# Optimization experiments

Hardware: AMD Instinct MI355X
Metric: run time of the kernel (lower is better)

Reference implementation:

```python
import jax, jax.numpy as jnp
import numpy as np

DIM = 1536; NH = 12; HD = 128; C2 = HD // 2          # rope half-dim = 64
F, H, W = 1, 30, 52
FRAME = H * W                                         # 1560 tokens/frame
SINK_FRAMES = 1; LOCAL_ATTN = 6
SINK = SINK_FRAMES * FRAME                            # 1560
MAX_ATTN = LOCAL_ATTN * 1560                          # 9360
CACHE = 9360                                          # kv cache length
GLOBAL_END = 9360; LOCAL_END_CACHE = 9360             # cache state before step
SPLITS = (C2 - 2 * (C2 // 3), C2 // 3, C2 // 3)       # (22, 21, 21)
EPS = 1e-6


def setup_inputs() -> dict:
    key = jax.random.key(0)
    ks = jax.random.split(key, 12)
    s = F * H * W
    rn = lambda k, sh, sc=1.0: jax.random.normal(k, sh, jnp.float32) * sc
    x = rn(ks[0], (1, s, DIM))
    Wq = rn(ks[1], (DIM, DIM), 0.02); Wk = rn(ks[2], (DIM, DIM), 0.02)
    Wv = rn(ks[3], (DIM, DIM), 0.02); Wo = rn(ks[4], (DIM, DIM), 0.02)
    zb = jnp.zeros((DIM,), jnp.float32)
    angles = jax.random.uniform(ks[5], (1024, C2), jnp.float32) * (2.0 * np.pi)
    freqs_cos = jnp.cos(angles); freqs_sin = jnp.sin(angles)
    cache_k = rn(ks[6], (1, CACHE, NH, HD)); cache_v = rn(ks[7], (1, CACHE, NH, HD))
    return dict(x=x, Wq=Wq, bq=zb, Wk=Wk, bk=zb, Wv=Wv, bv=zb, Wo=Wo, bo=zb,
                nq_w=jnp.ones((DIM,), jnp.float32), nk_w=jnp.ones((DIM,), jnp.float32),
                cache_k=cache_k, cache_v=cache_v,
                freqs_cos=freqs_cos, freqs_sin=freqs_sin,
                seq_lens=jnp.array([s], jnp.int32),
                grid_sizes=jnp.array([[F, H, W]], jnp.int32),
                current_start=GLOBAL_END)


def _rmsnorm(x, w):
    return x * jax.lax.rsqrt(jnp.mean(x * x, -1, keepdims=True) + EPS) * w


def _grid_table(table, start_frame):
    """table [1024, C2] -> per-token rope factors [S, 1, C2] over the (F,H,W) grid."""
    s0, s1, s2 = SPLITS
    tf, th, tw = table[:, :s0], table[:, s0:s0 + s1], table[:, s0 + s1:]
    fp = jnp.broadcast_to(tf[start_frame:start_frame + F][:, None, None, :], (F, H, W, s0))
    hp = jnp.broadcast_to(th[:H][None, :, None, :], (F, H, W, s1))
    wp = jnp.broadcast_to(tw[:W][None, None, :, :], (F, H, W, s2))
    return jnp.concatenate([fp, hp, wp], -1).reshape(F * H * W, 1, C2)


def _rope(x, cos, sin):
    # x: [b, s, n, d]; cos/sin: [s, 1, C2] (complex multiply in real arithmetic)
    b, s, n, d = x.shape
    xp = x.reshape(b, s, n, d // 2, 2)
    xr, xi = xp[..., 0], xp[..., 1]
    c, sn = cos[None], sin[None]                      # [1, s, 1, C2]
    out_r = xr * c - xi * sn
    out_i = xr * sn + xi * c
    return jnp.stack([out_r, out_i], -1).reshape(b, s, n, d)


def reference(x, Wq, bq, Wk, bk, Wv, bv, Wo, bo, nq_w, nk_w,
              cache_k, cache_v, freqs_cos, freqs_sin,
              seq_lens, grid_sizes, current_start):
    b, s = x.shape[:2]
    q = _rmsnorm(x @ Wq.T + bq, nq_w).reshape(b, s, NH, HD)
    k = _rmsnorm(x @ Wk.T + bk, nk_w).reshape(b, s, NH, HD)
    v = (x @ Wv.T + bv).reshape(b, s, NH, HD)

    start_frame = int(current_start) // FRAME
    cos = _grid_table(freqs_cos, start_frame)
    sin = _grid_table(freqs_sin, start_frame)
    rq = _rope(q, cos, sin)
    rk = _rope(k, cos, sin)

    # --- static cache bookkeeping (roll_and_insert path; all Python ints) ---
    num_new = s
    current_end = int(current_start) + num_new
    num_evicted = num_new + LOCAL_END_CACHE - CACHE           # 1560
    num_rolled = LOCAL_END_CACHE - num_evicted - SINK         # 6240
    local_end = LOCAL_END_CACHE + current_end - GLOBAL_END - num_evicted  # 9360
    local_start = local_end - num_new                         # 7800 == SINK + num_rolled
    temp_k = jnp.concatenate(
        [cache_k[:, :SINK], cache_k[:, SINK + num_evicted:SINK + num_evicted + num_rolled], rk], axis=1)
    temp_v = jnp.concatenate(
        [cache_v[:, :SINK], cache_v[:, SINK + num_evicted:SINK + num_evicted + num_rolled], v], axis=1)

    # --- sink + sliding-window attention ---
    local_budget = MAX_ATTN - SINK
    win_start = max(SINK, local_end - local_budget)
    k_cat = jnp.concatenate([temp_k[:, :SINK], temp_k[:, win_start:local_end]], axis=1)
    v_cat = jnp.concatenate([temp_v[:, :SINK], temp_v[:, win_start:local_end]], axis=1)

    logits = jnp.einsum('bqhd,bkhd->bhqk', rq, k_cat) * (HD ** -0.5)
    probs = jax.nn.softmax(logits, axis=-1)
    out = jnp.einsum('bhqk,bkhd->bqhd', probs, v_cat)
    y = out.reshape(b, s, DIM) @ Wo.T + bo
    return y
```

## Files before the change

kernel.cpp:

```cpp
#include <hip/hip_runtime.h>
#include <hip/hip_bf16.h>

typedef __bf16 bf16;
typedef __bf16 bf16x2 __attribute__((ext_vector_type(2)));
typedef __bf16 bf16x4 __attribute__((ext_vector_type(4)));
typedef __bf16 bf16x8 __attribute__((ext_vector_type(8)));
typedef float f32x4 __attribute__((ext_vector_type(4)));

#define DIM 1536
#define NH 12
#define HD 128
#define SEQ 1560
#define KV 9360
#define KVP 9408
#define SINK 1560
#define NEWBASE 7800
#define QSCALE 0.08838834764831845f
#define NSPLIT 3
#define CHUNK 3136

__device__ __forceinline__ void gl_lds16(const void* g, void* l) {
  __builtin_amdgcn_global_load_lds(
      (const __attribute__((address_space(1))) unsigned int*)g,
      (__attribute__((address_space(3))) unsigned int*)l, 16, 0, 0);
}

__global__ __launch_bounds__(256) void castk(const float* __restrict__ src,
                                             bf16* __restrict__ dst, int n) {
  int i = (blockIdx.x * 256 + threadIdx.x) * 8;
  if (i < n) {
    float4 a = *(const float4*)(src + i);
    float4 b = *(const float4*)(src + i + 4);
    bf16x8 o;
    o[0] = (bf16)a.x; o[1] = (bf16)a.y; o[2] = (bf16)a.z; o[3] = (bf16)a.w;
    o[4] = (bf16)b.x; o[5] = (bf16)b.y; o[6] = (bf16)b.z; o[7] = (bf16)b.w;
    *(bf16x8*)(dst + i) = o;
  }
}

struct GemmBatch {
  const bf16* B[3];
  const float* bias[3];
  float* C[3];
};

#define BM 128
#define BN 128
#define BK 32

__global__ __launch_bounds__(256, 2) void gemm_bt(const bf16* __restrict__ A,
                                                  GemmBatch gb, int M) {
  const bf16* Bw = gb.B[blockIdx.z];
  const float* bias = gb.bias[blockIdx.z];
  float* C = gb.C[blockIdx.z];
  int bm = blockIdx.x * BM;
  int bn = blockIdx.y * BN;

  __shared__ bf16 Alds[2][BM][BK];
  __shared__ bf16 Blds[2][BN][BK];

  int t = threadIdx.x;
  int lane = t & 63;
  int wave = t >> 6;
  int wr = wave >> 1, wc = wave & 1;
  int fr = lane & 15;
  int fo = (lane >> 4) * 8;

  f32x4 acc[4][4] = {};

  const int NK = DIM / BK;
  int colA = (lane & 3) * 8;
  int lrow = lane >> 2;

#define STAGE(buf, k0)                                                      \
  {                                                                         \
    _Pragma("unroll") for (int p = 0; p < 2; ++p) {                         \
      int rbase = wave * 16 + p * 64;                                       \
      int ga = bm + rbase + lrow;                                           \
      if (ga > M - 1) ga = M - 1;                                           \
      gl_lds16(A + (size_t)ga * DIM + (k0) + colA, &Alds[buf][rbase][0]);   \
      int gbv = bn + rbase + lrow;                                          \
      gl_lds16(Bw + (size_t)gbv * DIM + (k0) + colA, &Blds[buf][rbase][0]); \
    }                                                                       \
  }

  STAGE(0, 0);
  int cur = 0;
  for (int ks = 0; ks < NK; ++ks) {
    __syncthreads();
    if (ks + 1 < NK) STAGE(cur ^ 1, (ks + 1) * BK);
    bf16x8 af[4], bfv[4];
#pragma unroll
    for (int i = 0; i < 4; ++i)
      af[i] = *(const bf16x8*)&Alds[cur][wr * 64 + i * 16 + fr][fo];
#pragma unroll
    for (int j = 0; j < 4; ++j)
      bfv[j] = *(const bf16x8*)&Blds[cur][wc * 64 + j * 16 + fr][fo];
#pragma unroll
    for (int i = 0; i < 4; ++i)
#pragma unroll
      for (int j = 0; j < 4; ++j)
        acc[i][j] = __builtin_amdgcn_mfma_f32_16x16x32_bf16(af[i], bfv[j],
                                                            acc[i][j], 0, 0, 0);
    cur ^= 1;
  }
#undef STAGE

  int g4 = (lane >> 4) * 4;
#pragma unroll
  for (int i = 0; i < 4; ++i) {
    int mbase = bm + wr * 64 + i * 16 + g4;
#pragma unroll
    for (int j = 0; j < 4; ++j) {
      int col = bn + wc * 64 + j * 16 + fr;
      float bv = bias[col];
#pragma unroll
      for (int r = 0; r < 4; ++r) {
        int m = mbase + r;
        if (m < M) C[(size_t)m * DIM + col] = acc[i][j][r] + bv;
      }
    }
  }
}

__global__ __launch_bounds__(256) void norm_rope(
    const float* __restrict__ qraw, const float* __restrict__ kraw,
    const float* __restrict__ nqw, const float* __restrict__ nkw,
    const float* __restrict__ fcos, const float* __restrict__ fsin,
    bf16* __restrict__ Qh, bf16* __restrict__ Kcat) {
  int tok = blockIdx.x;
  int tid = threadIdx.x;
  const float* qr = qraw + (size_t)tok * DIM;
  const float* kr = kraw + (size_t)tok * DIM;
  float sq = 0.f, sk = 0.f;
  for (int c = tid; c < DIM; c += 256) {
    float a = qr[c];
    sq += a * a;
    float b = kr[c];
    sk += b * b;
  }
#pragma unroll
  for (int off = 32; off; off >>= 1) {
    sq += __shfl_down(sq, off);
    sk += __shfl_down(sk, off);
  }
  __shared__ float red[2][4];
  int w = tid >> 6;
  if ((tid & 63) == 0) {
    red[0][w] = sq;
    red[1][w] = sk;
  }
  __syncthreads();
  sq = red[0][0] + red[0][1] + red[0][2] + red[0][3];
  sk = red[1][0] + red[1][1] + red[1][2] + red[1][3];
  float rsq = rsqrtf(sq * (1.0f / DIM) + 1e-6f);
  float rsk = rsqrtf(sk * (1.0f / DIM) + 1e-6f);

  int hrow = tok / 52, wrow = tok % 52;
  for (int p = tid; p < NH * 64; p += 256) {
    int n = p >> 6, i = p & 63;
    int trow = (i < 22) ? 6 : (i < 43 ? hrow : wrow);
    float cs = fcos[trow * 64 + i];
    float sn = fsin[trow * 64 + i];
    int c = n * HD + 2 * i;
    float xr = qr[c] * rsq * nqw[c];
    float xi = qr[c + 1] * rsq * nqw[c + 1];
    bf16x2 qo;
    qo[0] = (bf16)((xr * cs - xi * sn) * QSCALE);
    qo[1] = (bf16)((xr * sn + xi * cs) * QSCALE);
    *(bf16x2*)(Qh + ((size_t)n * SEQ + tok) * HD + 2 * i) = qo;
    float yr = kr[c] * rsk * nkw[c];
    float yi = kr[c + 1] * rsk * nkw[c + 1];
    bf16x2 ko;
    ko[0] = (bf16)(yr * cs - yi * sn);
    ko[1] = (bf16)(yr * sn + yi * cs);
    *(bf16x2*)(Kcat + ((size_t)n * KVP + NEWBASE + tok) * HD + 2 * i) = ko;
  }
}

__global__ __launch_bounds__(256) void build_kcat(const float* __restrict__ cache_k,
                                                  bf16* __restrict__ Kcat) {
  int j = blockIdx.x;
  int src = j < SINK ? j : j + SINK;
  const float* sp = cache_k + (size_t)src * DIM;
  for (int c4 = threadIdx.x; c4 < DIM / 4; c4 += 256) {
    float4 v = *(const float4*)(sp + c4 * 4);
    int c = c4 * 4;
    int n = c >> 7, d = c & 127;
    bf16x4 o;
    o[0] = (bf16)v.x; o[1] = (bf16)v.y; o[2] = (bf16)v.z; o[3] = (bf16)v.w;
    *(bf16x4*)(Kcat + ((size_t)n * KVP + j) * HD + d) = o;
  }
}

__global__ __launch_bounds__(256) void build_vt(const float* __restrict__ cache_v,
                                                const float* __restrict__ vraw,
                                                bf16* __restrict__ Vt) {
  int h = blockIdx.y;
  int j0 = blockIdx.x * 64;
  __shared__ bf16 T[128][72];
  int tid = threadIdx.x;
  for (int idx = tid; idx < 64 * 32; idx += 256) {
    int jl = idx >> 5, s = idx & 31;
    int j = j0 + jl;
    if (j >= KV) continue;
    const float* sp;
    if (j < NEWBASE) {
      int srcj = j < SINK ? j : j + SINK;
      sp = cache_v + (size_t)srcj * DIM + h * HD;
    } else {
      sp = vraw + (size_t)(j - NEWBASE) * DIM + h * HD;
    }
    float4 v = *(const float4*)(sp + s * 4);
    T[s * 4 + 0][jl] = (bf16)v.x;
    T[s * 4 + 1][jl] = (bf16)v.y;
    T[s * 4 + 2][jl] = (bf16)v.z;
    T[s * 4 + 3][jl] = (bf16)v.w;
  }
  __syncthreads();
  for (int idx = tid; idx < 128 * 16; idx += 256) {
    int d = idx >> 4, g = idx & 15;
    int j = j0 + g * 4;
    if (j + 4 > KV) continue;
    bf16x4 o;
    o[0] = T[d][4 * g];
    o[1] = T[d][4 * g + 1];
    o[2] = T[d][4 * g + 2];
    o[3] = T[d][4 * g + 3];
    *(bf16x4*)(Vt + ((size_t)h * HD + d) * KVP + j) = o;
  }
}

__global__ __launch_bounds__(256, 4) void attn_split(const bf16* __restrict__ Qh,
                                                     const bf16* __restrict__ Kcat,
                                                     const bf16* __restrict__ Vt,
                                                     float* __restrict__ Opart,
                                                     float* __restrict__ MLpart) {
  int orig = blockIdx.x;
  int xcd = orig & 7, jj = orig >> 3;
  int wgid = (xcd < 4 ? xcd * 113 : 452 + (xcd - 4) * 112) + jj;
  int qt = wgid % 25;
  int h = (wgid / 25) % NH;
  int sp = wgid / 300;
  int q0 = qt * 64;
  int c0 = sp * CHUNK;

  int t = threadIdx.x, lane = t & 63, w = t >> 6;
  int g = lane >> 4, fr = lane & 15, s3 = fr & 7;

  __shared__ bf16 Klds[64][128];
  __shared__ bf16 Vlds[128][64];
  __shared__ bf16 Plds[4][16][64];

  int qrow = q0 + w * 16 + fr;
  int qcl = qrow < SEQ ? qrow : SEQ - 1;
  const bf16* Qp = Qh + ((size_t)h * SEQ + qcl) * HD + g * 8;
  bf16x8 qf[4];
#pragma unroll
  for (int fk = 0; fk < 4; ++fk) qf[fk] = *(const bf16x8*)(Qp + 32 * fk);

  int kadd[4], vadd[4];
#pragma unroll
  for (int p = 0; p < 4; ++p) {
    int m = (4 * w + p) * 64 + lane;
    int rK = m >> 4, cK = m & 15;
    kadd[p] = rK * HD + (cK ^ (rK & 7)) * 8;
    int dV = m >> 3, cV = m & 7;
    vadd[p] = dV * KVP + (cV ^ (dV & 7)) * 8;
  }
  char* KldsB = (char*)&Klds[0][0] + w * 4096;
  char* VldsB = (char*)&Vlds[0][0] + w * 4096;

  int koffr[4], voffc[2], poffc[2], pwb[4];
#pragma unroll
  for (int fk = 0; fk < 4; ++fk) koffr[fk] = fr * 256 + (((g + 4 * fk) ^ s3) * 16);
#pragma unroll
  for (int c = 0; c < 2; ++c) {
    voffc[c] = fr * 128 + (((g + 4 * c) ^ s3) * 16);
    poffc[c] = fr * 128 + (((4 * c + g) ^ s3) * 16);
  }
#pragma unroll
  for (int fj = 0; fj < 4; ++fj)
    pwb[fj] = fr * 128 + (((2 * fj + (g >> 1)) ^ s3) * 16) + (g & 1) * 8;
  char* PldsB = (char*)&Plds[w][0][0];

  const bf16* Khp = Kcat + (size_t)h * KVP * HD;
  const bf16* Vhp = Vt + (size_t)h * HD * KVP;

  f32x4 oacc[8] = {};
  float m_q = -1e30f, l_q = 0.f;

  for (int j0 = c0; j0 < c0 + CHUNK; j0 += 64) {
    __syncthreads();
    const bf16* Ks = Khp + (size_t)j0 * HD;
    const bf16* Vs = Vhp + j0;
#pragma unroll
    for (int p = 0; p < 4; ++p) gl_lds16(Ks + kadd[p], KldsB + p * 1024);
#pragma unroll
    for (int p = 0; p < 4; ++p) gl_lds16(Vs + vadd[p], VldsB + p * 1024);
    __syncthreads();

    f32x4 sacc[4] = {};
    __builtin_amdgcn_s_setprio(1);
#pragma unroll
    for (int fj = 0; fj < 4; ++fj)
#pragma unroll
      for (int fk = 0; fk < 4; ++fk) {
        bf16x8 kf = *(const bf16x8*)((const char*)&Klds[0][0] + fj * 4096 + koffr[fk]);
        sacc[fj] = __builtin_amdgcn_mfma_f32_16x16x32_bf16(kf, qf[fk], sacc[fj], 0, 0, 0);
      }
    __builtin_amdgcn_s_setprio(0);

    if (j0 + 64 > KV) {
#pragma unroll
      for (int fj = 0; fj < 4; ++fj)
#pragma unroll
        for (int r = 0; r < 4; ++r)
          if (j0 + 16 * fj + 4 * g + r >= KV) sacc[fj][r] = -1e30f;
    }

    float mx = sacc[0][0];
#pragma unroll
    for (int fj = 0; fj < 4; ++fj)
#pragma unroll
      for (int r = 0; r < 4; ++r)
        if (fj | r) mx = fmaxf(mx, sacc[fj][r]);
    mx = fmaxf(mx, __shfl_xor(mx, 16));
    mx = fmaxf(mx, __shfl_xor(mx, 32));
    float mnew = fmaxf(m_q, mx);
    float corr = __expf(m_q - mnew);
    m_q = mnew;
    float sum = 0.f;
    bf16x4 pw[4];
#pragma unroll
    for (int fj = 0; fj < 4; ++fj)
#pragma unroll
      for (int r = 0; r < 4; ++r) {
        float e = __expf(sacc[fj][r] - mnew);
        pw[fj][r] = (bf16)e;
        sum += e;
      }
    sum += __shfl_xor(sum, 16);
    sum += __shfl_xor(sum, 32);
    l_q = l_q * corr + sum;

    float corr_r[4];
#pragma unroll
    for (int r = 0; r < 4; ++r) corr_r[r] = __shfl(corr, 4 * g + r);
#pragma unroll
    for (int fd = 0; fd < 8; ++fd)
#pragma unroll
      for (int r = 0; r < 4; ++r) oacc[fd][r] *= corr_r[r];

#pragma unroll
    for (int fj = 0; fj < 4; ++fj) *(bf16x4*)(PldsB + pwb[fj]) = pw[fj];

    bf16x8 pa0 = *(const bf16x8*)(PldsB + poffc[0]);
    bf16x8 pa1 = *(const bf16x8*)(PldsB + poffc[1]);
    __builtin_amdgcn_s_setprio(1);
#pragma unroll
    for (int fd = 0; fd < 8; ++fd) {
      bf16x8 v0 = *(const bf16x8*)((const char*)&Vlds[0][0] + fd * 2048 + voffc[0]);
      bf16x8 v1 = *(const bf16x8*)((const char*)&Vlds[0][0] + fd * 2048 + voffc[1]);
      oacc[fd] = __builtin_amdgcn_mfma_f32_16x16x32_bf16(pa0, v0, oacc[fd], 0, 0, 0);
      oacc[fd] = __builtin_amdgcn_mfma_f32_16x16x32_bf16(pa1, v1, oacc[fd], 0, 0, 0);
    }
    __builtin_amdgcn_s_setprio(0);
  }

  float* Oh = Opart + ((size_t)sp * NH + h) * SEQ * HD;
  float* MLh = MLpart + ((size_t)sp * NH + h) * SEQ * 2;
#pragma unroll
  for (int r = 0; r < 4; ++r) {
    int q = q0 + w * 16 + 4 * g + r;
    if (q >= SEQ) continue;
#pragma unroll
    for (int fd = 0; fd < 8; ++fd)
      Oh[(size_t)q * HD + fr + 16 * fd] = oacc[fd][r];
  }
  if (lane < 16) {
    int q = q0 + w * 16 + lane;
    if (q < SEQ) {
      MLh[q * 2 + 0] = m_q;
      MLh[q * 2 + 1] = l_q;
    }
  }
}

__global__ __launch_bounds__(256) void attn_merge(const float* __restrict__ Opart,
                                                  const float* __restrict__ MLpart,
                                                  bf16* __restrict__ Aout) {
  int idx = blockIdx.x * 2 + (threadIdx.x >> 7);
  if (idx >= NH * SEQ) return;
  int d = threadIdx.x & 127;
  int h = idx / SEQ, q = idx % SEQ;
  float m[NSPLIT];
  float M = -1e30f;
#pragma unroll
  for (int s = 0; s < NSPLIT; ++s) {
    m[s] = MLpart[(((size_t)s * NH + h) * SEQ + q) * 2];
    M = fmaxf(M, m[s]);
  }
  float L = 0.f, o = 0.f;
#pragma unroll
  for (int s = 0; s < NSPLIT; ++s) {
    float wgt = __expf(m[s] - M);
    L += MLpart[(((size_t)s * NH + h) * SEQ + q) * 2 + 1] * wgt;
    o += Opart[((((size_t)s * NH + h) * SEQ + q)) * HD + d] * wgt;
  }
  Aout[(size_t)q * DIM + h * HD + d] = (bf16)(o / L);
}

extern "C" void kernel_launch(void* const* d_in, const int* in_sizes, int n_in,
                              void* d_out, int out_size, void* d_ws, size_t ws_size,
                              hipStream_t stream) {
  const float* x = (const float*)d_in[0];
  const float* Wq = (const float*)d_in[1];
  const float* bq = (const float*)d_in[2];
  const float* Wk = (const float*)d_in[3];
  const float* bk = (const float*)d_in[4];
  const float* Wv = (const float*)d_in[5];
  const float* bv = (const float*)d_in[6];
  const float* Wo = (const float*)d_in[7];
  const float* bo = (const float*)d_in[8];
  const float* nqw = (const float*)d_in[9];
  const float* nkw = (const float*)d_in[10];
  const float* cache_k = (const float*)d_in[11];
  const float* cache_v = (const float*)d_in[12];
  const float* fcos = (const float*)d_in[13];
  const float* fsin = (const float*)d_in[14];
  float* out = (float*)d_out;

  char* ws = (char*)d_ws;
  size_t off = 0;
  auto alloc = [&](size_t bytes) {
    char* p = ws + off;
    off += (bytes + 255) & ~(size_t)255;
    return p;
  };
  const int XN = SEQ * DIM;
  const int WN = DIM * DIM;
  bf16* xb = (bf16*)alloc((size_t)XN * 2);
  bf16* Wqb = (bf16*)alloc((size_t)WN * 2);
  bf16* Wkb = (bf16*)alloc((size_t)WN * 2);
  bf16* Wvb = (bf16*)alloc((size_t)WN * 2);
  bf16* Wob = (bf16*)alloc((size_t)WN * 2);
  float* qraw = (float*)alloc((size_t)XN * 4);
  float* kraw = (float*)alloc((size_t)XN * 4);
  float* vraw = (float*)alloc((size_t)XN * 4);
  bf16* QhB = (bf16*)alloc((size_t)NH * SEQ * HD * 2);
  bf16* Kcat = (bf16*)alloc((size_t)NH * KVP * HD * 2);
  bf16* Vt = (bf16*)alloc((size_t)NH * HD * KVP * 2);
  bf16* Aout = (bf16*)alloc((size_t)XN * 2);
  float* Opart = (float*)alloc((size_t)NSPLIT * NH * SEQ * HD * 4);
  float* MLpart = (float*)alloc((size_t)NSPLIT * NH * SEQ * 2 * 4);

  castk<<<(XN + 2047) / 2048, 256, 0, stream>>>(x, xb, XN);
  castk<<<(WN + 2047) / 2048, 256, 0, stream>>>(Wq, Wqb, WN);
  castk<<<(WN + 2047) / 2048, 256, 0, stream>>>(Wk, Wkb, WN);
  castk<<<(WN + 2047) / 2048, 256, 0, stream>>>(Wv, Wvb, WN);
  castk<<<(WN + 2047) / 2048, 256, 0, stream>>>(Wo, Wob, WN);

  GemmBatch gqkv;
  gqkv.B[0] = Wqb; gqkv.B[1] = Wkb; gqkv.B[2] = Wvb;
  gqkv.bias[0] = bq; gqkv.bias[1] = bk; gqkv.bias[2] = bv;
  gqkv.C[0] = qraw; gqkv.C[1] = kraw; gqkv.C[2] = vraw;
  gemm_bt<<<dim3(13, 12, 3), 256, 0, stream>>>(xb, gqkv, SEQ);

  norm_rope<<<SEQ, 256, 0, stream>>>(qraw, kraw, nqw, nkw, fcos, fsin, QhB, Kcat);
  build_kcat<<<NEWBASE, 256, 0, stream>>>(cache_k, Kcat);
  build_vt<<<dim3(147, NH), 256, 0, stream>>>(cache_v, vraw, Vt);

  attn_split<<<dim3(25 * NH * NSPLIT), 256, 0, stream>>>(QhB, Kcat, Vt, Opart, MLpart);
  attn_merge<<<(NH * SEQ + 1) / 2, 256, 0, stream>>>(Opart, MLpart, Aout);

  GemmBatch gout;
  gout.B[0] = Wob; gout.B[1] = Wob; gout.B[2] = Wob;
  gout.bias[0] = bo; gout.bias[1] = bo; gout.bias[2] = bo;
  gout.C[0] = out; gout.C[1] = out; gout.C[2] = out;
  gemm_bt<<<dim3(13, 12, 1), 256, 0, stream>>>(Aout, gout, SEQ);
}
```

Baseline: 332.1 us.

## Double query tile per attention block and double-buffer K/V LDS loads

```diff
diff --git a/kernel.cpp b/kernel.cpp
--- a/kernel.cpp
+++ b/kernel.cpp
@@ -18,6 +18,9 @@
 #define QSCALE 0.08838834764831845f
 #define NSPLIT 3
 #define CHUNK 3136
+#define NT 49
+#define QBLK 128
+#define NQT 13
 
 __device__ __forceinline__ void gl_lds16(const void* g, void* l) {
   __builtin_amdgcn_global_load_lds(
@@ -72,7 +75,7 @@
   int colA = (lane & 3) * 8;
   int lrow = lane >> 2;
 
-#define STAGE(buf, k0)                                                      \
+#define STAGEG(buf, k0)                                                     \
   {                                                                         \
     _Pragma("unroll") for (int p = 0; p < 2; ++p) {                         \
       int rbase = wave * 16 + p * 64;                                       \
@@ -84,11 +87,11 @@
     }                                                                       \
   }
 
-  STAGE(0, 0);
+  STAGEG(0, 0);
   int cur = 0;
   for (int ks = 0; ks < NK; ++ks) {
     __syncthreads();
-    if (ks + 1 < NK) STAGE(cur ^ 1, (ks + 1) * BK);
+    if (ks + 1 < NK) STAGEG(cur ^ 1, (ks + 1) * BK);
     bf16x8 af[4], bfv[4];
 #pragma unroll
     for (int i = 0; i < 4; ++i)
@@ -104,7 +107,7 @@
                                                             acc[i][j], 0, 0, 0);
     cur ^= 1;
   }
-#undef STAGE
+#undef STAGEG
 
   int g4 = (lane >> 4) * 4;
 #pragma unroll
@@ -231,33 +234,36 @@
   }
 }
 
-__global__ __launch_bounds__(256, 4) void attn_split(const bf16* __restrict__ Qh,
+__global__ __launch_bounds__(256, 2) void attn_split(const bf16* __restrict__ Qh,
                                                      const bf16* __restrict__ Kcat,
                                                      const bf16* __restrict__ Vt,
                                                      float* __restrict__ Opart,
                                                      float* __restrict__ MLpart) {
   int orig = blockIdx.x;
   int xcd = orig & 7, jj = orig >> 3;
-  int wgid = (xcd < 4 ? xcd * 113 : 452 + (xcd - 4) * 112) + jj;
-  int qt = wgid % 25;
-  int h = (wgid / 25) % NH;
-  int sp = wgid / 300;
-  int q0 = qt * 64;
+  int wgid = (xcd < 4 ? xcd * 59 : 236 + (xcd - 4) * 58) + jj;
+  int qt = wgid % NQT;
+  int h = (wgid / NQT) % NH;
+  int sp = wgid / (NQT * NH);
+  int q0 = qt * QBLK;
   int c0 = sp * CHUNK;
 
   int t = threadIdx.x, lane = t & 63, w = t >> 6;
   int g = lane >> 4, fr = lane & 15, s3 = fr & 7;
 
-  __shared__ bf16 Klds[64][128];
-  __shared__ bf16 Vlds[128][64];
-  __shared__ bf16 Plds[4][16][64];
-
-  int qrow = q0 + w * 16 + fr;
-  int qcl = qrow < SEQ ? qrow : SEQ - 1;
-  const bf16* Qp = Qh + ((size_t)h * SEQ + qcl) * HD + g * 8;
-  bf16x8 qf[4];
-#pragma unroll
-  for (int fk = 0; fk < 4; ++fk) qf[fk] = *(const bf16x8*)(Qp + 32 * fk);
+  __shared__ bf16 Klds[2][64][128];
+  __shared__ bf16 Vlds[2][128][64];
+  __shared__ bf16 Plds[4][2][16][64];
+
+  bf16x8 qf[2][4];
+#pragma unroll
+  for (int s = 0; s < 2; ++s) {
+    int qrow = q0 + w * 32 + s * 16 + fr;
+    int qcl = qrow < SEQ ? qrow : SEQ - 1;
+    const bf16* Qp = Qh + ((size_t)h * SEQ + qcl) * HD + g * 8;
+#pragma unroll
+    for (int fk = 0; fk < 4; ++fk) qf[s][fk] = *(const bf16x8*)(Qp + 32 * fk);
+  }
 
   int kadd[4], vadd[4];
 #pragma unroll
@@ -268,8 +274,8 @@
     int dV = m >> 3, cV = m & 7;
     vadd[p] = dV * KVP + (cV ^ (dV & 7)) * 8;
   }
-  char* KldsB = (char*)&Klds[0][0] + w * 4096;
-  char* VldsB = (char*)&Vlds[0][0] + w * 4096;
+  char* Kbase = (char*)&Klds[0][0][0];
+  char* Vbase = (char*)&Vlds[0][0][0];
 
   int koffr[4], voffc[2], poffc[2], pwb[4];
 #pragma unroll
@@ -282,32 +288,46 @@
 #pragma unroll
   for (int fj = 0; fj < 4; ++fj)
     pwb[fj] = fr * 128 + (((2 * fj + (g >> 1)) ^ s3) * 16) + (g & 1) * 8;
-  char* PldsB = (char*)&Plds[w][0][0];
+  char* PldsB0 = (char*)&Plds[w][0][0][0];
+  char* PldsB1 = (char*)&Plds[w][1][0][0];
 
   const bf16* Khp = Kcat + (size_t)h * KVP * HD;
   const bf16* Vhp = Vt + (size_t)h * HD * KVP;
 
-  f32x4 oacc[8] = {};
-  float m_q = -1e30f, l_q = 0.f;
-
-  for (int j0 = c0; j0 < c0 + CHUNK; j0 += 64) {
-    __syncthreads();
-    const bf16* Ks = Khp + (size_t)j0 * HD;
-    const bf16* Vs = Vhp + j0;
-#pragma unroll
-    for (int p = 0; p < 4; ++p) gl_lds16(Ks + kadd[p], KldsB + p * 1024);
-#pragma unroll
-    for (int p = 0; p < 4; ++p) gl_lds16(Vs + vadd[p], VldsB + p * 1024);
-    __syncthreads();
-
-    f32x4 sacc[4] = {};
+  f32x4 oacc[2][8] = {};
+  float m_q[2] = {-1e30f, -1e30f};
+  float l_q[2] = {0.f, 0.f};
+
+#define STAGE(buf, j0)                                                   \
+  {                                                                      \
+    const bf16* Ks = Khp + (size_t)(j0)*HD;                              \
+    const bf16* Vs = Vhp + (j0);                                         \
+    _Pragma("unroll") for (int p = 0; p < 4; ++p)                        \
+        gl_lds16(Ks + kadd[p], Kbase + (buf)*16384 + w * 4096 + p * 1024); \
+    _Pragma("unroll") for (int p = 0; p < 4; ++p)                        \
+        gl_lds16(Vs + vadd[p], Vbase + (buf)*16384 + w * 4096 + p * 1024); \
+  }
+
+  STAGE(0, c0);
+  __syncthreads();
+  int cur = 0;
+
+  for (int ti = 0; ti < NT; ++ti) {
+    int j0 = c0 + ti * 64;
+    if (ti + 1 < NT) STAGE(cur ^ 1, j0 + 64);
+
+    const char* Kc = Kbase + cur * 16384;
+    const char* Vc = Vbase + cur * 16384;
+
+    f32x4 sacc[2][4] = {};
     __builtin_amdgcn_s_setprio(1);
 #pragma unroll
     for (int fj = 0; fj < 4; ++fj)
 #pragma unroll
       for (int fk = 0; fk < 4; ++fk) {
-        bf16x8 kf = *(const bf16x8*)((const char*)&Klds[0][0] + fj * 4096 + koffr[fk]);
-        sacc[fj] = __builtin_amdgcn_mfma_f32_16x16x32_bf16(kf, qf[fk], sacc[fj], 0, 0, 0);
+        bf16x8 kf = *(const bf16x8*)(Kc + fj * 4096 + koffr[fk]);
+        sacc[0][fj] = __builtin_amdgcn_mfma_f32_16x16x32_bf16(kf, qf[0][fk], sacc[0][fj], 0, 0, 0);
+        sacc[1][fj] = __builtin_amdgcn_mfma_f32_16x16x32_bf16(kf, qf[1][fk], sacc[1][fj], 0, 0, 0);
       }
     __builtin_amdgcn_s_setprio(0);
 
@@ -316,73 +336,96 @@
       for (int fj = 0; fj < 4; ++fj)
 #pragma unroll
         for (int r = 0; r < 4; ++r)
-          if (j0 + 16 * fj + 4 * g + r >= KV) sacc[fj][r] = -1e30f;
-    }
-
-    float mx = sacc[0][0];
-#pragma unroll
-    for (int fj = 0; fj < 4; ++fj)
-#pragma unroll
-      for (int r = 0; r < 4; ++r)
-        if (fj | r) mx = fmaxf(mx, sacc[fj][r]);
-    mx = fmaxf(mx, __shfl_xor(mx, 16));
-    mx = fmaxf(mx, __shfl_xor(mx, 32));
-    float mnew = fmaxf(m_q, mx);
-    float corr = __expf(m_q - mnew);
-    m_q = mnew;
-    float sum = 0.f;
-    bf16x4 pw[4];
-#pragma unroll
-    for (int fj = 0; fj < 4; ++fj)
-#pragma unroll
-      for (int r = 0; r < 4; ++r) {
-        float e = __expf(sacc[fj][r] - mnew);
-        pw[fj][r] = (bf16)e;
-        sum += e;
-      }
-    sum += __shfl_xor(sum, 16);
-    sum += __shfl_xor(sum, 32);
-    l_q = l_q * corr + sum;
-
-    float corr_r[4];
-#pragma unroll
-    for (int r = 0; r < 4; ++r) corr_r[r] = __shfl(corr, 4 * g + r);
-#pragma unroll
-    for (int fd = 0; fd < 8; ++fd)
-#pragma unroll
-      for (int r = 0; r < 4; ++r) oacc[fd][r] *= corr_r[r];
-
-#pragma unroll
-    for (int fj = 0; fj < 4; ++fj) *(bf16x4*)(PldsB + pwb[fj]) = pw[fj];
-
-    bf16x8 pa0 = *(const bf16x8*)(PldsB + poffc[0]);
-    bf16x8 pa1 = *(const bf16x8*)(PldsB + poffc[1]);
+          if (j0 + 16 * fj + 4 * g + r >= KV) {
+            sacc[0][fj][r] = -1e30f;
+            sacc[1][fj][r] = -1e30f;
+          }
+    }
+
+#pragma unroll
+    for (int s = 0; s < 2; ++s) {
+      float mx = sacc[s][0][0];
+#pragma unroll
+      for (int fj = 0; fj < 4; ++fj)
+#pragma unroll
+        for (int r = 0; r < 4; ++r)
+          if (fj | r) mx = fmaxf(mx, sacc[s][fj][r]);
+      mx = fmaxf(mx, __shfl_xor(mx, 16));
+      mx = fmaxf(mx, __shfl_xor(mx, 32));
+      float mnew = fmaxf(m_q[s], mx);
+      float corr = __expf(m_q[s] - mnew);
+      m_q[s] = mnew;
+      float sum = 0.f;
+      bf16x4 pw[4];
+#pragma unroll
+      for (int fj = 0; fj < 4; ++fj)
+#pragma unroll
+        for (int r = 0; r < 4; ++r) {
+          float e = __expf(sacc[s][fj][r] - mnew);
+          pw[fj][r] = (bf16)e;
+          sum += e;
+        }
+      sum += __shfl_xor(sum, 16);
+      sum += __shfl_xor(sum, 32);
+      l_q[s] = l_q[s] * corr + sum;
+
+      float corr_r[4];
+#pragma unroll
+      for (int r = 0; r < 4; ++r) corr_r[r] = __shfl(corr, 4 * g + r);
+#pragma unroll
+      for (int fd = 0; fd < 8; ++fd)
+#pragma unroll
+        for (int r = 0; r < 4; ++r) oacc[s][fd][r] *= corr_r[r];
+
+      char* PB = s ? PldsB1 : PldsB0;
+#pragma unroll
+      for (int fj = 0; fj < 4; ++fj) *(bf16x4*)(PB + pwb[fj]) = pw[fj];
+    }
+
+    bf16x8 pa[2][2];
+#pragma unroll
+    for (int c = 0; c < 2; ++c) {
+      pa[0][c] = *(const bf16x8*)(PldsB0 + poffc[c]);
+      pa[1][c] = *(const bf16x8*)(PldsB1 + poffc[c]);
+    }
     __builtin_amdgcn_s_setprio(1);
 #pragma unroll
     for (int fd = 0; fd < 8; ++fd) {
-      bf16x8 v0 = *(const bf16x8*)((const char*)&Vlds[0][0] + fd * 2048 + voffc[0]);
-      bf16x8 v1 = *(const bf16x8*)((const char*)&Vlds[0][0] + fd * 2048 + voffc[1]);
-      oacc[fd] = __builtin_amdgcn_mfma_f32_16x16x32_bf16(pa0, v0, oacc[fd], 0, 0, 0);
-      oacc[fd] = __builtin_amdgcn_mfma_f32_16x16x32_bf16(pa1, v1, oacc[fd], 0, 0, 0);
+      bf16x8 v0 = *(const bf16x8*)(Vc + fd * 2048 + voffc[0]);
+      bf16x8 v1 = *(const bf16x8*)(Vc + fd * 2048 + voffc[1]);
+      oacc[0][fd] = __builtin_amdgcn_mfma_f32_16x16x32_bf16(pa[0][0], v0, oacc[0][fd], 0, 0, 0);
+      oacc[0][fd] = __builtin_amdgcn_mfma_f32_16x16x32_bf16(pa[0][1], v1, oacc[0][fd], 0, 0, 0);
+      oacc[1][fd] = __builtin_amdgcn_mfma_f32_16x16x32_bf16(pa[1][0], v0, oacc[1][fd], 0, 0, 0);
+      oacc[1][fd] = __builtin_amdgcn_mfma_f32_16x16x32_bf16(pa[1][1], v1, oacc[1][fd], 0, 0, 0);
     }
     __builtin_amdgcn_s_setprio(0);
-  }
+
+    __syncthreads();
+    cur ^= 1;
+  }
+#undef STAGE
 
   float* Oh = Opart + ((size_t)sp * NH + h) * SEQ * HD;
   float* MLh = MLpart + ((size_t)sp * NH + h) * SEQ * 2;
 #pragma unroll
-  for (int r = 0; r < 4; ++r) {
-    int q = q0 + w * 16 + 4 * g + r;
-    if (q >= SEQ) continue;
-#pragma unroll
-    for (int fd = 0; fd < 8; ++fd)
-      Oh[(size_t)q * HD + fr + 16 * fd] = oacc[fd][r];
+  for (int s = 0; s < 2; ++s) {
+#pragma unroll
+    for (int r = 0; r < 4; ++r) {
+      int q = q0 + w * 32 + s * 16 + 4 * g + r;
+      if (q >= SEQ) continue;
+#pragma unroll
+      for (int fd = 0; fd < 8; ++fd)
+        Oh[(size_t)q * HD + fr + 16 * fd] = oacc[s][fd][r];
+    }
   }
   if (lane < 16) {
-    int q = q0 + w * 16 + lane;
-    if (q < SEQ) {
-      MLh[q * 2 + 0] = m_q;
-      MLh[q * 2 + 1] = l_q;
+#pragma unroll
+    for (int s = 0; s < 2; ++s) {
+      int q = q0 + w * 32 + s * 16 + lane;
+      if (q < SEQ) {
+        MLh[q * 2 + 0] = m_q[s];
+        MLh[q * 2 + 1] = l_q[s];
+      }
     }
   }
 }
@@ -471,7 +514,7 @@
   build_kcat<<<NEWBASE, 256, 0, stream>>>(cache_k, Kcat);
   build_vt<<<dim3(147, NH), 256, 0, stream>>>(cache_v, vraw, Vt);
 
-  attn_split<<<dim3(25 * NH * NSPLIT), 256, 0, stream>>>(QhB, Kcat, Vt, Opart, MLpart);
+  attn_split<<<dim3(NQT * NH * NSPLIT), 256, 0, stream>>>(QhB, Kcat, Vt, Opart, MLpart);
   attn_merge<<<(NH * SEQ + 1) / 2, 256, 0, stream>>>(Opart, MLpart, Aout);
 
   GemmBatch gout;
```

Result: faster. 305.9 us (-7.9%).
